# Optimization experiments

Measured on AMD Instinct MI355X. Metric: run time of the kernel, lower is better.

Reference implementation:

```python
import jax, jax.numpy as jnp
import numpy as np

B, S, H, L, NH, FF, V, NL = 16, 512, 768, 12, 12, 3072, 30522, 9
DH = H // NH


def setup_inputs() -> dict:
    key = jax.random.key(0)
    ks = iter(jax.random.split(key, 16))
    def w(shape, scale=0.02):
        return jax.random.normal(next(ks), shape, jnp.float32) * scale
    return {
        "input_word_ids": jax.random.randint(next(ks), (B, S), 0, V, jnp.int32),
        "input_mask": jnp.ones((B, S), jnp.int32),
        "input_type_ids": jnp.zeros((B, S), jnp.int32),
        "valid_mask": jax.random.randint(next(ks), (B, S), 0, 2, jnp.int32),
        "word_emb": w((V, H)),
        "pos_emb": w((S, H)),
        "type_emb": w((2, H)),
        "emb_ln_g": jnp.ones((H,), jnp.float32),
        "emb_ln_b": jnp.zeros((H,), jnp.float32),
        "Wq": w((L, H, H)), "bq": jnp.zeros((L, H), jnp.float32),
        "Wk": w((L, H, H)), "bk": jnp.zeros((L, H), jnp.float32),
        "Wv": w((L, H, H)), "bv": jnp.zeros((L, H), jnp.float32),
        "Wo": w((L, H, H)), "bo": jnp.zeros((L, H), jnp.float32),
        "ln1_g": jnp.ones((L, H), jnp.float32), "ln1_b": jnp.zeros((L, H), jnp.float32),
        "W1": w((L, H, FF)), "b1": jnp.zeros((L, FF), jnp.float32),
        "W2": w((L, FF, H)), "b2": jnp.zeros((L, H), jnp.float32),
        "ln2_g": jnp.ones((L, H), jnp.float32), "ln2_b": jnp.zeros((L, H), jnp.float32),
        "cls_W": w((H, NL)), "cls_b": jnp.zeros((NL,), jnp.float32),
    }


def _layer_norm(x, g, b):
    m = x.mean(-1, keepdims=True)
    v = ((x - m) ** 2).mean(-1, keepdims=True)
    return (x - m) * jax.lax.rsqrt(v + 1e-12) * g + b


def reference(input_word_ids, input_mask, input_type_ids, valid_mask,
              word_emb, pos_emb, type_emb, emb_ln_g, emb_ln_b,
              Wq, bq, Wk, bk, Wv, bv, Wo, bo, ln1_g, ln1_b,
              W1, b1, W2, b2, ln2_g, ln2_b, cls_W, cls_b):
    b, s = input_word_ids.shape
    # --- BERT embeddings ---
    x = word_emb[input_word_ids] + pos_emb[None, :s] + type_emb[input_type_ids]
    x = _layer_norm(x, emb_ln_g, emb_ln_b)  # [B,S,H]
    attn_bias = (1.0 - input_mask.astype(jnp.float32))[:, None, None, :] * -1e9
    scale = 1.0 / np.sqrt(DH).astype(np.float32)

    def step(h, p):
        wq, bq_, wk, bk_, wv, bv_, wo, bo_, g1, gb1, w1, wb1, w2, wb2, g2, gb2 = p
        q = (h @ wq + bq_).reshape(b, s, NH, DH)
        k = (h @ wk + bk_).reshape(b, s, NH, DH)
        v = (h @ wv + bv_).reshape(b, s, NH, DH)
        scores = jnp.einsum('bqhd,bkhd->bhqk', q, k) * scale + attn_bias
        probs = jax.nn.softmax(scores, axis=-1)
        ctx = jnp.einsum('bhqk,bkhd->bqhd', probs, v).reshape(b, s, H)
        h = _layer_norm(h + ctx @ wo + bo_, g1, gb1)
        ff = jax.nn.gelu(h @ w1 + wb1, approximate=False)
        h = _layer_norm(h + ff @ w2 + wb2, g2, gb2)
        return h, None

    params = (Wq, bq, Wk, bk, Wv, bv, Wo, bo, ln1_g, ln1_b, W1, b1, W2, b2, ln2_g, ln2_b)
    x, _ = jax.lax.scan(step, x, params)

    # --- valid-token compaction (vectorized form of the python double loop) ---
    # valid tokens packed to the front (stable order), remainder zero-padded
    invalid = (1 - valid_mask).astype(jnp.int32)
    perm = jnp.argsort(invalid, axis=1, stable=True)          # [B,S]
    compact = jnp.take_along_axis(x, perm[:, :, None], axis=1)
    counts = valid_mask.sum(axis=1)                           # [B]
    keep = (jnp.arange(s)[None, :] < counts[:, None])[:, :, None]
    compact = jnp.where(keep, compact, jnp.zeros((), x.dtype))
    # dropout is identity at inference (training=False)
    logits = jax.nn.softmax(compact @ cls_W + cls_b, axis=-1)  # [B,S,NL]
    return logits
```

## Files before the change

### kernel.cpp

```cpp
#include <hip/hip_runtime.h>
#include <cstdint>
#include <cstddef>

#define B_ 16
#define S_ 512
#define H_ 768
#define L_ 12
#define NH_ 12
#define DH_ 64
#define FF_ 3072
#define NL_ 9
#define QKV_ 2304

typedef _Float16 f16x8 __attribute__((ext_vector_type(8)));
typedef _Float16 f16x4 __attribute__((ext_vector_type(4)));
typedef float f32x4 __attribute__((ext_vector_type(4)));

__device__ __forceinline__ void load_lds16(const void* g, void* l) {
  __builtin_amdgcn_global_load_lds(
      (const __attribute__((address_space(1))) unsigned int*)g,
      (__attribute__((address_space(3))) unsigned int*)l, 16, 0, 0);
}

__device__ __forceinline__ float block_sum256(float v, float* red) {
#pragma unroll
  for (int off = 32; off; off >>= 1) v += __shfl_down(v, off);
  __syncthreads();
  if ((threadIdx.x & 63) == 0) red[threadIdx.x >> 6] = v;
  __syncthreads();
  return red[0] + red[1] + red[2] + red[3];
}

__device__ __forceinline__ float block_sum192(float v, float* red) {
#pragma unroll
  for (int off = 32; off; off >>= 1) v += __shfl_down(v, off);
  __syncthreads();
  if ((threadIdx.x & 63) == 0) red[threadIdx.x >> 6] = v;
  __syncthreads();
  return red[0] + red[1] + red[2];
}

__device__ __forceinline__ float gelu_f(float x) {
  float au = fabsf(x) * 0.70710678118654752f;
  float t = 1.0f / (1.0f + 0.3275911f * au);
  float p = ((((1.061405429f * t - 1.453152027f) * t + 1.421413741f) * t
              - 0.284496736f) * t + 0.254829592f) * t;
  float e = p * __expf(-au * au);
  float phi = (x >= 0.0f) ? (1.0f - 0.5f * e) : (0.5f * e);
  return x * phi;
}

__global__ __launch_bounds__(256) void embed_ln_kernel(
    const int* __restrict__ wid, const int* __restrict__ tpid,
    const float* __restrict__ we, const float* __restrict__ pe,
    const float* __restrict__ te, const float* __restrict__ g,
    const float* __restrict__ bb, _Float16* __restrict__ hb) {
  __shared__ float red[4];
  int tok = blockIdx.x;
  int s = tok & (S_ - 1);
  int w = wid[tok], tp = tpid[tok];
  int t = threadIdx.x;
  float x[3];
#pragma unroll
  for (int i = 0; i < 3; ++i) {
    int j = t + i * 256;
    x[i] = we[(size_t)w * H_ + j] + pe[(size_t)s * H_ + j] + te[(size_t)tp * H_ + j];
  }
  float m = block_sum256(x[0] + x[1] + x[2], red) * (1.0f / H_);
  float d0 = x[0] - m, d1 = x[1] - m, d2 = x[2] - m;
  float var = block_sum256(d0 * d0 + d1 * d1 + d2 * d2, red) * (1.0f / H_);
  float rs = rsqrtf(var + 1e-12f);
#pragma unroll
  for (int i = 0; i < 3; ++i) {
    int j = t + i * 256;
    float v = (x[i] - m) * rs * g[j] + bb[j];
    hb[(size_t)tok * H_ + j] = (_Float16)v;
  }
}

__global__ __launch_bounds__(192) void ln_f16_kernel(
    const _Float16* __restrict__ x, const float* __restrict__ g,
    const float* __restrict__ bb, _Float16* __restrict__ hb) {
  __shared__ float red[3];
  int tok = blockIdx.x;
  int t = threadIdx.x;
  int j = t * 4;
  f16x4 xv = *(const f16x4*)&x[(size_t)tok * H_ + j];
  float v0 = (float)xv[0], v1 = (float)xv[1], v2 = (float)xv[2], v3 = (float)xv[3];
  float m = block_sum192(v0 + v1 + v2 + v3, red) * (1.0f / H_);
  float d0 = v0 - m, d1 = v1 - m, d2 = v2 - m, d3 = v3 - m;
  __syncthreads();
  float var = block_sum192(d0 * d0 + d1 * d1 + d2 * d2 + d3 * d3, red) * (1.0f / H_);
  float rs = rsqrtf(var + 1e-12f);
  float4 gv = *(const float4*)&g[j];
  float4 bv = *(const float4*)&bb[j];
  f16x4 o;
  o[0] = (_Float16)(d0 * rs * gv.x + bv.x);
  o[1] = (_Float16)(d1 * rs * gv.y + bv.y);
  o[2] = (_Float16)(d2 * rs * gv.z + bv.z);
  o[3] = (_Float16)(d3 * rs * gv.w + bv.w);
  *(f16x4*)&hb[(size_t)tok * H_ + j] = o;
}

__global__ __launch_bounds__(256) void convert_weights_kernel(
    const float* __restrict__ Wq, const float* __restrict__ Wk,
    const float* __restrict__ Wv, const float* __restrict__ Wo,
    const float* __restrict__ W1, const float* __restrict__ W2,
    _Float16* __restrict__ qT, _Float16* __restrict__ kT,
    _Float16* __restrict__ vT, _Float16* __restrict__ oT,
    _Float16* __restrict__ w1T, _Float16* __restrict__ w2T,
    const float* __restrict__ bq, const float* __restrict__ bk,
    const float* __restrict__ bv, float* __restrict__ qkvb) {
  int id = blockIdx.x;
  int tid = threadIdx.x;
  if (id == 1728) {
    for (int j = tid; j < H_; j += 256) {
      qkvb[j] = bq[j];
      qkvb[H_ + j] = bk[j];
      qkvb[2 * H_ + j] = bv[j];
    }
    return;
  }
  __shared__ float T[64][65];
  const float* src;
  _Float16* dst;
  int K, N, tk, tn;
  if (id < 576) {
    int mat = id / 144, t = id % 144;
    K = 768; N = 768; tk = t / 12; tn = t % 12;
    src = (mat == 0) ? Wq : (mat == 1) ? Wk : (mat == 2) ? Wv : Wo;
    dst = (mat == 0) ? qT : (mat == 1) ? kT : (mat == 2) ? vT : oT;
  } else if (id < 1152) {
    int t = id - 576; K = 768; N = 3072; tk = t / 48; tn = t % 48;
    src = W1; dst = w1T;
  } else {
    int t = id - 1152; K = 3072; N = 768; tk = t / 12; tn = t % 12;
    src = W2; dst = w2T;
  }
  int k0 = tk * 64, n0 = tn * 64;
  {
    int r = tid >> 4, c4 = (tid & 15) * 4;
#pragma unroll
    for (int i = 0; i < 4; ++i) {
      float4 v = *(const float4*)&src[(size_t)(k0 + r + i * 16) * N + n0 + c4];
      T[r + i * 16][c4 + 0] = v.x;
      T[r + i * 16][c4 + 1] = v.y;
      T[r + i * 16][c4 + 2] = v.z;
      T[r + i * 16][c4 + 3] = v.w;
    }
  }
  __syncthreads();
#pragma unroll
  for (int i = 0; i < 2; ++i) {
    int chunk = tid + i * 256;
    int n = chunk >> 3, kc = (chunk & 7) * 8;
    f16x8 o;
#pragma unroll
    for (int j = 0; j < 8; ++j) o[j] = (_Float16)T[kc + j][n];
    *(f16x8*)&dst[(size_t)(n0 + n) * K + k0 + kc] = o;
  }
}

template <int OUT>
__global__ __launch_bounds__(256) void gemm_f16(
    const _Float16* __restrict__ A, const _Float16* __restrict__ Bt,
    const float* __restrict__ bias, void* __restrict__ Cv,
    int M, int N, int K, const _Float16* __restrict__ hres) {
  __shared__ _Float16 As[2][128 * 64];
  __shared__ _Float16 Bs[2][128 * 64];
  int tid = threadIdx.x;
  int lane = tid & 63, w = tid >> 6;
  int wr = w >> 1, wc = w & 1;
  int l15 = lane & 15, kb = lane >> 4;
  int swr = l15 & 7;

  int nwg = gridDim.x * gridDim.y;
  int bid = blockIdx.y * gridDim.x + blockIdx.x;
  int swz = bid;
  if ((nwg & 7) == 0) {
    int cpx = nwg >> 3;
    swz = (bid & 7) * cpx + (bid >> 3);
  }
  int bx = swz % gridDim.x, by = swz / gridDim.x;
  int row0 = by * 128, col0 = bx * 128;

  int drow = lane >> 3;
  int schunk = (lane & 7) ^ drow;
  const _Float16* gA = A + (size_t)(row0 + w * 32 + drow) * K + schunk * 8;
  const _Float16* gB = Bt + (size_t)(col0 + w * 32 + drow) * K + schunk * 8;

  auto STAGE = [&](int t, int buf) {
    int ko = t * 64;
#pragma unroll
    for (int j = 0; j < 4; ++j) {
      load_lds16(gA + (size_t)(j * 8) * K + ko,
                 (char*)&As[buf][0] + (w * 32 + j * 8) * 128);
      load_lds16(gB + (size_t)(j * 8) * K + ko,
                 (char*)&Bs[buf][0] + (w * 32 + j * 8) * 128);
    }
  };

  f32x4 acc[4][4] = {};
  int nk = K >> 6;

  STAGE(0, 0);
  __syncthreads();

  for (int kt = 0; kt < nk; ++kt) {
    int cur = kt & 1;
    if (kt + 1 < nk) STAGE(kt + 1, cur ^ 1);
#pragma unroll
    for (int ks = 0; ks < 2; ++ks) {
      f16x8 af[4], bf[4];
      int rpos = ((ks * 4 + kb) ^ swr) * 8;
#pragma unroll
      for (int m = 0; m < 4; ++m)
        af[m] = *(const f16x8*)&As[cur][(wr * 64 + m * 16 + l15) * 64 + rpos];
#pragma unroll
      for (int n = 0; n < 4; ++n)
        bf[n] = *(const f16x8*)&Bs[cur][(wc * 64 + n * 16 + l15) * 64 + rpos];
#pragma unroll
      for (int m = 0; m < 4; ++m)
#pragma unroll
        for (int n = 0; n < 4; ++n)
          acc[m][n] = __builtin_amdgcn_mfma_f32_16x16x32_f16(af[m], bf[n], acc[m][n], 0, 0, 0);
    }
    __syncthreads();
  }
#pragma unroll
  for (int n = 0; n < 4; ++n) {
    int col = col0 + wc * 64 + n * 16 + l15;
    float bv = bias[col];
#pragma unroll
    for (int m = 0; m < 4; ++m) {
      int rowb = row0 + wr * 64 + m * 16 + kb * 4;
#pragma unroll
      for (int r = 0; r < 4; ++r) {
        float v = acc[m][n][r] + bv;
        if (OUT == 2) v = gelu_f(v);
        if (OUT == 3) v += (float)hres[(size_t)(rowb + r) * N + col];
        ((_Float16*)Cv)[(size_t)(rowb + r) * N + col] = (_Float16)v;
      }
    }
  }
}

__global__ __launch_bounds__(256) void vtrans_kernel(
    const _Float16* __restrict__ v, int RS, _Float16* __restrict__ vt) {
  __shared__ _Float16 T[64][72];
  int s0 = blockIdx.x * 64;
  int bh = blockIdx.y;
  int b = bh / NH_, h = bh % NH_;
  int tid = threadIdx.x;
#pragma unroll
  for (int i = 0; i < 2; ++i) {
    int chunk = tid + i * 256;
    int s = chunk >> 3, dc = (chunk & 7) * 8;
    *(f16x8*)&T[s][dc] = *(const f16x8*)&v[(size_t)(b * S_ + s0 + s) * RS + h * DH_ + dc];
  }
  __syncthreads();
#pragma unroll
  for (int i = 0; i < 2; ++i) {
    int chunk = tid + i * 256;
    int d = chunk >> 3, sc = (chunk & 7) * 8;
    f16x8 o;
#pragma unroll
    for (int j = 0; j < 8; ++j) o[j] = T[sc + j][d];
    *(f16x8*)&vt[(size_t)(bh * DH_ + d) * S_ + s0 + sc] = o;
  }
}

__global__ __launch_bounds__(256) void flash_attn_kernel(
    const _Float16* __restrict__ q, const _Float16* __restrict__ k,
    const _Float16* __restrict__ vt, int RS, const int* __restrict__ mask,
    _Float16* __restrict__ ctx) {
  __shared__ _Float16 Ks[128 * 72];
  __shared__ _Float16 Vs[64 * 136];
  __shared__ _Float16 Ps[4][16 * 136];
  __shared__ float biasz[S_];
  int qt = blockIdx.x, h = blockIdx.y, b = blockIdx.z;
  int tid = threadIdx.x, lane = tid & 63, w = tid >> 6;
  int l15 = lane & 15, kb = lane >> 4;
  const float C = 0.125f * 1.44269504088896f;

  for (int i = tid; i < S_; i += 256)
    biasz[i] = (1.0f - (float)mask[b * S_ + i]) * (-1e9f * C);

  int qrow = b * S_ + qt * 64 + w * 16 + l15;
  f16x8 qf[2];
  qf[0] = *(const f16x8*)&q[(size_t)qrow * RS + h * DH_ + kb * 8];
  qf[1] = *(const f16x8*)&q[(size_t)qrow * RS + h * DH_ + 32 + kb * 8];

  auto loadKV = [&](int kt, f16x8* rk, f16x8* rv) {
#pragma unroll
    for (int i = 0; i < 4; ++i) {
      int idx = tid + i * 256;
      int r = idx >> 3, c = idx & 7;
      rk[i] = *(const f16x8*)&k[(size_t)(b * S_ + kt * 128 + r) * RS + h * DH_ + c * 8];
      int d = idx >> 4, c2 = idx & 15;
      rv[i] = *(const f16x8*)&vt[(size_t)((b * NH_ + h) * DH_ + d) * S_ + kt * 128 + c2 * 8];
    }
  };

  float m_run[4], l_run[4];
  f32x4 o[4] = {};
#pragma unroll
  for (int r = 0; r < 4; ++r) { m_run[r] = -1e30f; l_run[r] = 0.f; }

  f16x8 rk[4], rv[4];
  loadKV(0, rk, rv);
  for (int kt = 0; kt < 4; ++kt) {
    __syncthreads();
#pragma unroll
    for (int i = 0; i < 4; ++i) {
      int idx = tid + i * 256;
      int r = idx >> 3, c = idx & 7;
      *(f16x8*)&Ks[r * 72 + c * 8] = rk[i];
      int d = idx >> 4, c2 = idx & 15;
      *(f16x8*)&Vs[d * 136 + c2 * 8] = rv[i];
    }
    __syncthreads();
    if (kt < 3) loadKV(kt + 1, rk, rv);
    f32x4 s[8];
#pragma unroll
    for (int nf = 0; nf < 8; ++nf) {
      f16x8 b0 = *(const f16x8*)&Ks[(nf * 16 + l15) * 72 + kb * 8];
      f16x8 b1 = *(const f16x8*)&Ks[(nf * 16 + l15) * 72 + 32 + kb * 8];
      f32x4 z = {};
      z = __builtin_amdgcn_mfma_f32_16x16x32_f16(qf[0], b0, z, 0, 0, 0);
      z = __builtin_amdgcn_mfma_f32_16x16x32_f16(qf[1], b1, z, 0, 0, 0);
      s[nf] = z;
    }
    float zb[8];
#pragma unroll
    for (int nf = 0; nf < 8; ++nf) zb[nf] = biasz[kt * 128 + nf * 16 + l15];
    float pw[8][4];
    float corr[4];
#pragma unroll
    for (int r = 0; r < 4; ++r) {
      float mx = -1e30f;
#pragma unroll
      for (int nf = 0; nf < 8; ++nf) mx = fmaxf(mx, s[nf][r] * C + zb[nf]);
#pragma unroll
      for (int d = 1; d < 16; d <<= 1) mx = fmaxf(mx, __shfl_xor(mx, d));
      float mnew = fmaxf(m_run[r], mx);
      float cr = exp2f(m_run[r] - mnew);
      m_run[r] = mnew;
      corr[r] = cr;
      float sum = 0.f;
#pragma unroll
      for (int nf = 0; nf < 8; ++nf) {
        float pv = exp2f(s[nf][r] * C + zb[nf] - mnew);
        pw[nf][r] = pv;
        sum += pv;
      }
#pragma unroll
      for (int d = 1; d < 16; d <<= 1) sum += __shfl_xor(sum, d);
      l_run[r] = l_run[r] * cr + sum;
    }
#pragma unroll
    for (int nf2 = 0; nf2 < 4; ++nf2)
#pragma unroll
      for (int r = 0; r < 4; ++r) o[nf2][r] *= corr[r];
#pragma unroll
    for (int nf = 0; nf < 8; ++nf)
#pragma unroll
      for (int r = 0; r < 4; ++r)
        Ps[w][(kb * 4 + r) * 136 + nf * 16 + l15] = (_Float16)pw[nf][r];
#pragma unroll
    for (int ks = 0; ks < 4; ++ks) {
      f16x8 pa = *(const f16x8*)&Ps[w][l15 * 136 + ks * 32 + kb * 8];
#pragma unroll
      for (int nf2 = 0; nf2 < 4; ++nf2) {
        f16x8 vb2 = *(const f16x8*)&Vs[(nf2 * 16 + l15) * 136 + ks * 32 + kb * 8];
        o[nf2] = __builtin_amdgcn_mfma_f32_16x16x32_f16(pa, vb2, o[nf2], 0, 0, 0);
      }
    }
  }
  float inv[4];
#pragma unroll
  for (int r = 0; r < 4; ++r) inv[r] = 1.0f / fmaxf(l_run[r], 1e-37f);
#pragma unroll
  for (int nf2 = 0; nf2 < 4; ++nf2)
#pragma unroll
    for (int r = 0; r < 4; ++r) {
      int row = b * S_ + qt * 64 + w * 16 + kb * 4 + r;
      ctx[(size_t)row * H_ + h * DH_ + nf2 * 16 + l15] = (_Float16)(o[nf2][r] * inv[r]);
    }
}

__global__ void compact_idx_kernel(const int* __restrict__ valid, int* __restrict__ dest) {
  int b = threadIdx.x;
  if (b >= B_) return;
  int cnt = 0;
  for (int s = 0; s < S_; ++s) {
    int vv = valid[b * S_ + s];
    dest[b * S_ + s] = vv ? cnt : -1;
    cnt += vv;
  }
}

__global__ __launch_bounds__(192) void scatter_kernel(
    const _Float16* __restrict__ hb, const int* __restrict__ dest,
    float* __restrict__ compact) {
  int tok = blockIdx.x;
  int d = dest[tok];
  if (d < 0) return;
  int b = tok >> 9;
  int j = threadIdx.x * 4;
  f16x4 v = *(const f16x4*)&hb[(size_t)tok * H_ + j];
  float4 o = {(float)v[0], (float)v[1], (float)v[2], (float)v[3]};
  *(float4*)&compact[((size_t)(b * S_ + d)) * H_ + j] = o;
}

__global__ __launch_bounds__(256) void cls_kernel(
    const float* __restrict__ x, const float* __restrict__ W,
    const float* __restrict__ bias2, float* __restrict__ out) {
  int lane = threadIdx.x & 63, wv = threadIdx.x >> 6;
  int tok = blockIdx.x * 4 + wv;
  float acc[NL_] = {};
  for (int hh = lane; hh < H_; hh += 64) {
    float xv = x[(size_t)tok * H_ + hh];
#pragma unroll
    for (int n = 0; n < NL_; ++n) acc[n] = fmaf(xv, W[hh * NL_ + n], acc[n]);
  }
#pragma unroll
  for (int n = 0; n < NL_; ++n) {
#pragma unroll
    for (int off = 32; off; off >>= 1) acc[n] += __shfl_down(acc[n], off);
  }
  if (lane == 0) {
    float vls[NL_], mx = -1e30f;
#pragma unroll
    for (int n = 0; n < NL_; ++n) {
      vls[n] = acc[n] + bias2[n];
      mx = fmaxf(mx, vls[n]);
    }
    float s = 0.f;
#pragma unroll
    for (int n = 0; n < NL_; ++n) {
      vls[n] = expf(vls[n] - mx);
      s += vls[n];
    }
    float inv = 1.0f / s;
#pragma unroll
    for (int n = 0; n < NL_; ++n) out[(size_t)tok * NL_ + n] = vls[n] * inv;
  }
}

extern "C" void kernel_launch(void* const* d_in, const int* in_sizes, int n_in,
                              void* d_out, int out_size, void* d_ws, size_t ws_size,
                              hipStream_t stream) {
  const int* wid = (const int*)d_in[0];
  const int* mask = (const int*)d_in[1];
  const int* tpid = (const int*)d_in[2];
  const int* valid = (const int*)d_in[3];
  const float* we = (const float*)d_in[4];
  const float* pe = (const float*)d_in[5];
  const float* te = (const float*)d_in[6];
  const float* eg = (const float*)d_in[7];
  const float* eb = (const float*)d_in[8];
  const float* Wq = (const float*)d_in[9];
  const float* bq = (const float*)d_in[10];
  const float* Wk = (const float*)d_in[11];
  const float* bk = (const float*)d_in[12];
  const float* Wv = (const float*)d_in[13];
  const float* bv = (const float*)d_in[14];
  const float* Wo = (const float*)d_in[15];
  const float* bo = (const float*)d_in[16];
  const float* g1 = (const float*)d_in[17];
  const float* gb1 = (const float*)d_in[18];
  const float* W1 = (const float*)d_in[19];
  const float* bf1 = (const float*)d_in[20];
  const float* W2 = (const float*)d_in[21];
  const float* bf2 = (const float*)d_in[22];
  const float* g2 = (const float*)d_in[23];
  const float* gb2 = (const float*)d_in[24];
  const float* cW = (const float*)d_in[25];
  const float* cb = (const float*)d_in[26];
  float* out = (float*)d_out;

  const size_t TOK = (size_t)B_ * S_;
  char* ws = (char*)d_ws;
  _Float16* hb = (_Float16*)(ws + 25165824);
  _Float16* t1h = (_Float16*)(ws + 37748736);
  char* un1 = ws + 62914560;
  _Float16* qkv = (_Float16*)un1;
  _Float16* vt = (_Float16*)(un1 + 37748736);
  _Float16* ffh = (_Float16*)un1;
  float* compactf = (float*)un1;
  _Float16* ctx = (_Float16*)(ws + 113246208);
  char* wbuf = ws + 125829120;
  _Float16* wqT = (_Float16*)wbuf;
  _Float16* wkT = (_Float16*)(wbuf + 1179648);
  _Float16* wvT = (_Float16*)(wbuf + 2359296);
  _Float16* woT = (_Float16*)(wbuf + 3538944);
  _Float16* w1T = (_Float16*)(wbuf + 4718592);
  _Float16* w2T = (_Float16*)(wbuf + 9437184);
  int* dest = (int*)(ws + 139984896);
  float* qkvb = (float*)(ws + 140017664);

  dim3 blk(256);
  dim3 blk192(192);
  embed_ln_kernel<<<dim3((unsigned)TOK), blk, 0, stream>>>(wid, tpid, we, pe, te, eg, eb, hb);

  dim3 gQKV(QKV_ / 128, TOK / 128);
  dim3 gH(H_ / 128, TOK / 128);
  dim3 gF(FF_ / 128, TOK / 128);
  for (int l = 0; l < L_; ++l) {
    convert_weights_kernel<<<dim3(1729), blk, 0, stream>>>(
        Wq + (size_t)l * H_ * H_, Wk + (size_t)l * H_ * H_,
        Wv + (size_t)l * H_ * H_, Wo + (size_t)l * H_ * H_,
        W1 + (size_t)l * H_ * FF_, W2 + (size_t)l * FF_ * H_,
        wqT, wkT, wvT, woT, w1T, w2T,
        bq + l * H_, bk + l * H_, bv + l * H_, qkvb);
    gemm_f16<1><<<gQKV, blk, 0, stream>>>(hb, wqT, qkvb, qkv, (int)TOK, QKV_, H_, nullptr);
    vtrans_kernel<<<dim3(S_ / 64, B_ * NH_), blk, 0, stream>>>(qkv + 2 * H_, QKV_, vt);
    flash_attn_kernel<<<dim3(S_ / 64, NH_, B_), blk, 0, stream>>>(
        qkv, qkv + H_, vt, QKV_, mask, ctx);
    gemm_f16<3><<<gH, blk, 0, stream>>>(ctx, woT, bo + l * H_, t1h, (int)TOK, H_, H_, hb);
    ln_f16_kernel<<<dim3((unsigned)TOK), blk192, 0, stream>>>(t1h, g1 + l * H_, gb1 + l * H_, hb);
    gemm_f16<2><<<gF, blk, 0, stream>>>(hb, w1T, bf1 + l * FF_, ffh, (int)TOK, FF_, H_, nullptr);
    gemm_f16<3><<<gH, blk, 0, stream>>>(ffh, w2T, bf2 + l * H_, t1h, (int)TOK, H_, FF_, hb);
    ln_f16_kernel<<<dim3((unsigned)TOK), blk192, 0, stream>>>(t1h, g2 + l * H_, gb2 + l * H_, hb);
  }

  compact_idx_kernel<<<1, 64, 0, stream>>>(valid, dest);
  hipMemsetAsync(compactf, 0, TOK * H_ * sizeof(float), stream);
  scatter_kernel<<<dim3((unsigned)TOK), blk192, 0, stream>>>(hb, dest, compactf);
  cls_kernel<<<dim3((unsigned)(TOK / 4)), blk, 0, stream>>>(compactf, cW, cb, out);
}
```

Before: 3.431 ms.

## Use 64x128 GEMM tiles, precompute mask bias, fuse compaction into classifier gather

GEMM tiles shrink from 128x128 with 4 waves to 64x128 with 2 waves per block, each wave owning a 64-column slice. This doubles the grid size, which helps occupancy and tail behaviour, at the cost of less A/B reuse per block. The attention mask bias is now computed once by its own kernel instead of in every attention block. The final compaction drops the fp32 memset and scatter: the classifier reads each fp16 hidden row through a gather index and treats padded rows as zero.

```diff
diff --git a/kernel.cpp b/kernel.cpp
--- a/kernel.cpp
+++ b/kernel.cpp
@@ -14,6 +14,7 @@
 
 typedef _Float16 f16x8 __attribute__((ext_vector_type(8)));
 typedef _Float16 f16x4 __attribute__((ext_vector_type(4)));
+typedef _Float16 f16x2 __attribute__((ext_vector_type(2)));
 typedef float f32x4 __attribute__((ext_vector_type(4)));
 
 __device__ __forceinline__ void load_lds16(const void* g, void* l) {
@@ -161,16 +162,21 @@
   }
 }
 
+__global__ void maskbias_kernel(const int* __restrict__ mask, float* __restrict__ bz) {
+  int i = blockIdx.x * 256 + threadIdx.x;
+  const float C = 0.125f * 1.44269504088896f;
+  bz[i] = (1.0f - (float)mask[i]) * (-1e9f * C);
+}
+
 template <int OUT>
-__global__ __launch_bounds__(256) void gemm_f16(
+__global__ __launch_bounds__(128) void gemm64(
     const _Float16* __restrict__ A, const _Float16* __restrict__ Bt,
     const float* __restrict__ bias, void* __restrict__ Cv,
     int M, int N, int K, const _Float16* __restrict__ hres) {
-  __shared__ _Float16 As[2][128 * 64];
+  __shared__ _Float16 As[2][64 * 64];
   __shared__ _Float16 Bs[2][128 * 64];
   int tid = threadIdx.x;
   int lane = tid & 63, w = tid >> 6;
-  int wr = w >> 1, wc = w & 1;
   int l15 = lane & 15, kb = lane >> 4;
   int swr = l15 & 7;
 
@@ -182,22 +188,23 @@
     swz = (bid & 7) * cpx + (bid >> 3);
   }
   int bx = swz % gridDim.x, by = swz / gridDim.x;
-  int row0 = by * 128, col0 = bx * 128;
+  int row0 = by * 64, col0 = bx * 128;
 
   int drow = lane >> 3;
   int schunk = (lane & 7) ^ drow;
   const _Float16* gA = A + (size_t)(row0 + w * 32 + drow) * K + schunk * 8;
-  const _Float16* gB = Bt + (size_t)(col0 + w * 32 + drow) * K + schunk * 8;
+  const _Float16* gB = Bt + (size_t)(col0 + w * 64 + drow) * K + schunk * 8;
 
   auto STAGE = [&](int t, int buf) {
     int ko = t * 64;
 #pragma unroll
-    for (int j = 0; j < 4; ++j) {
+    for (int j = 0; j < 4; ++j)
       load_lds16(gA + (size_t)(j * 8) * K + ko,
                  (char*)&As[buf][0] + (w * 32 + j * 8) * 128);
+#pragma unroll
+    for (int j = 0; j < 8; ++j)
       load_lds16(gB + (size_t)(j * 8) * K + ko,
-                 (char*)&Bs[buf][0] + (w * 32 + j * 8) * 128);
-    }
+                 (char*)&Bs[buf][0] + (w * 64 + j * 8) * 128);
   };
 
   f32x4 acc[4][4] = {};
@@ -215,10 +222,10 @@
       int rpos = ((ks * 4 + kb) ^ swr) * 8;
 #pragma unroll
       for (int m = 0; m < 4; ++m)
-        af[m] = *(const f16x8*)&As[cur][(wr * 64 + m * 16 + l15) * 64 + rpos];
+        af[m] = *(const f16x8*)&As[cur][(m * 16 + l15) * 64 + rpos];
 #pragma unroll
       for (int n = 0; n < 4; ++n)
-        bf[n] = *(const f16x8*)&Bs[cur][(wc * 64 + n * 16 + l15) * 64 + rpos];
+        bf[n] = *(const f16x8*)&Bs[cur][(w * 64 + n * 16 + l15) * 64 + rpos];
 #pragma unroll
       for (int m = 0; m < 4; ++m)
 #pragma unroll
@@ -229,11 +236,11 @@
   }
 #pragma unroll
   for (int n = 0; n < 4; ++n) {
-    int col = col0 + wc * 64 + n * 16 + l15;
+    int col = col0 + w * 64 + n * 16 + l15;
     float bv = bias[col];
 #pragma unroll
     for (int m = 0; m < 4; ++m) {
-      int rowb = row0 + wr * 64 + m * 16 + kb * 4;
+      int rowb = row0 + m * 16 + kb * 4;
 #pragma unroll
       for (int r = 0; r < 4; ++r) {
         float v = acc[m][n][r] + bv;
@@ -272,7 +279,7 @@
 
 __global__ __launch_bounds__(256) void flash_attn_kernel(
     const _Float16* __restrict__ q, const _Float16* __restrict__ k,
-    const _Float16* __restrict__ vt, int RS, const int* __restrict__ mask,
+    const _Float16* __restrict__ vt, int RS, const float* __restrict__ biasz_g,
     _Float16* __restrict__ ctx) {
   __shared__ _Float16 Ks[128 * 72];
   __shared__ _Float16 Vs[64 * 136];
@@ -283,8 +290,7 @@
   int l15 = lane & 15, kb = lane >> 4;
   const float C = 0.125f * 1.44269504088896f;
 
-  for (int i = tid; i < S_; i += 256)
-    biasz[i] = (1.0f - (float)mask[b * S_ + i]) * (-1e9f * C);
+  for (int i = tid; i < S_; i += 256) biasz[i] = biasz_g[b * S_ + i];
 
   int qrow = b * S_ + qt * 64 + w * 16 + l15;
   f16x8 qf[2];
@@ -389,40 +395,31 @@
     }
 }
 
-__global__ void compact_idx_kernel(const int* __restrict__ valid, int* __restrict__ dest) {
+__global__ void compact_idx_kernel(const int* __restrict__ valid, int* __restrict__ src_of) {
   int b = threadIdx.x;
   if (b >= B_) return;
   int cnt = 0;
-  for (int s = 0; s < S_; ++s) {
-    int vv = valid[b * S_ + s];
-    dest[b * S_ + s] = vv ? cnt : -1;
-    cnt += vv;
-  }
-}
-
-__global__ __launch_bounds__(192) void scatter_kernel(
-    const _Float16* __restrict__ hb, const int* __restrict__ dest,
-    float* __restrict__ compact) {
-  int tok = blockIdx.x;
-  int d = dest[tok];
-  if (d < 0) return;
-  int b = tok >> 9;
-  int j = threadIdx.x * 4;
-  f16x4 v = *(const f16x4*)&hb[(size_t)tok * H_ + j];
-  float4 o = {(float)v[0], (float)v[1], (float)v[2], (float)v[3]};
-  *(float4*)&compact[((size_t)(b * S_ + d)) * H_ + j] = o;
+  for (int s = 0; s < S_; ++s)
+    if (valid[b * S_ + s]) src_of[b * S_ + cnt++] = b * S_ + s;
+  for (int d = cnt; d < S_; ++d) src_of[b * S_ + d] = -1;
 }
 
 __global__ __launch_bounds__(256) void cls_kernel(
-    const float* __restrict__ x, const float* __restrict__ W,
-    const float* __restrict__ bias2, float* __restrict__ out) {
+    const _Float16* __restrict__ hb, const int* __restrict__ src_of,
+    const float* __restrict__ W, const float* __restrict__ bias2,
+    float* __restrict__ out) {
   int lane = threadIdx.x & 63, wv = threadIdx.x >> 6;
   int tok = blockIdx.x * 4 + wv;
+  int src = src_of[tok];
   float acc[NL_] = {};
-  for (int hh = lane; hh < H_; hh += 64) {
-    float xv = x[(size_t)tok * H_ + hh];
-#pragma unroll
-    for (int n = 0; n < NL_; ++n) acc[n] = fmaf(xv, W[hh * NL_ + n], acc[n]);
+  if (src >= 0) {
+    for (int h0 = lane * 2; h0 < H_; h0 += 128) {
+      f16x2 xv = *(const f16x2*)&hb[(size_t)src * H_ + h0];
+      float x0 = (float)xv[0], x1 = (float)xv[1];
+#pragma unroll
+      for (int n = 0; n < NL_; ++n)
+        acc[n] = fmaf(x0, W[h0 * NL_ + n], fmaf(x1, W[(h0 + 1) * NL_ + n], acc[n]));
+    }
   }
 #pragma unroll
   for (int n = 0; n < NL_; ++n) {
@@ -488,7 +485,6 @@
   _Float16* qkv = (_Float16*)un1;
   _Float16* vt = (_Float16*)(un1 + 37748736);
   _Float16* ffh = (_Float16*)un1;
-  float* compactf = (float*)un1;
   _Float16* ctx = (_Float16*)(ws + 113246208);
   char* wbuf = ws + 125829120;
   _Float16* wqT = (_Float16*)wbuf;
@@ -497,16 +493,19 @@
   _Float16* woT = (_Float16*)(wbuf + 3538944);
   _Float16* w1T = (_Float16*)(wbuf + 4718592);
   _Float16* w2T = (_Float16*)(wbuf + 9437184);
-  int* dest = (int*)(ws + 139984896);
+  int* src_of = (int*)(ws + 139984896);
   float* qkvb = (float*)(ws + 140017664);
+  float* biasz_g = (float*)(ws + 140026880);
 
   dim3 blk(256);
   dim3 blk192(192);
+  dim3 blk128(128);
   embed_ln_kernel<<<dim3((unsigned)TOK), blk, 0, stream>>>(wid, tpid, we, pe, te, eg, eb, hb);
-
-  dim3 gQKV(QKV_ / 128, TOK / 128);
-  dim3 gH(H_ / 128, TOK / 128);
-  dim3 gF(FF_ / 128, TOK / 128);
+  maskbias_kernel<<<dim3((unsigned)(TOK / 256)), blk, 0, stream>>>(mask, biasz_g);
+
+  dim3 gQKV64(QKV_ / 128, TOK / 64);
+  dim3 gH64(H_ / 128, TOK / 64);
+  dim3 gF64(FF_ / 128, TOK / 64);
   for (int l = 0; l < L_; ++l) {
     convert_weights_kernel<<<dim3(1729), blk, 0, stream>>>(
         Wq + (size_t)l * H_ * H_, Wk + (size_t)l * H_ * H_,
@@ -514,19 +513,17 @@
         W1 + (size_t)l * H_ * FF_, W2 + (size_t)l * FF_ * H_,
         wqT, wkT, wvT, woT, w1T, w2T,
         bq + l * H_, bk + l * H_, bv + l * H_, qkvb);
-    gemm_f16<1><<<gQKV, blk, 0, stream>>>(hb, wqT, qkvb, qkv, (int)TOK, QKV_, H_, nullptr);
+    gemm64<1><<<gQKV64, blk128, 0, stream>>>(hb, wqT, qkvb, qkv, (int)TOK, QKV_, H_, nullptr);
     vtrans_kernel<<<dim3(S_ / 64, B_ * NH_), blk, 0, stream>>>(qkv + 2 * H_, QKV_, vt);
     flash_attn_kernel<<<dim3(S_ / 64, NH_, B_), blk, 0, stream>>>(
-        qkv, qkv + H_, vt, QKV_, mask, ctx);
-    gemm_f16<3><<<gH, blk, 0, stream>>>(ctx, woT, bo + l * H_, t1h, (int)TOK, H_, H_, hb);
+        qkv, qkv + H_, vt, QKV_, biasz_g, ctx);
+    gemm64<3><<<gH64, blk128, 0, stream>>>(ctx, woT, bo + l * H_, t1h, (int)TOK, H_, H_, hb);
     ln_f16_kernel<<<dim3((unsigned)TOK), blk192, 0, stream>>>(t1h, g1 + l * H_, gb1 + l * H_, hb);
-    gemm_f16<2><<<gF, blk, 0, stream>>>(hb, w1T, bf1 + l * FF_, ffh, (int)TOK, FF_, H_, nullptr);
-    gemm_f16<3><<<gH, blk, 0, stream>>>(ffh, w2T, bf2 + l * H_, t1h, (int)TOK, H_, FF_, hb);
+    gemm64<2><<<gF64, blk128, 0, stream>>>(hb, w1T, bf1 + l * FF_, ffh, (int)TOK, FF_, H_, nullptr);
+    gemm64<3><<<gH64, blk128, 0, stream>>>(ffh, w2T, bf2 + l * H_, t1h, (int)TOK, H_, FF_, hb);
     ln_f16_kernel<<<dim3((unsigned)TOK), blk192, 0, stream>>>(t1h, g2 + l * H_, gb2 + l * H_, hb);
   }
 
-  compact_idx_kernel<<<1, 64, 0, stream>>>(valid, dest);
-  hipMemsetAsync(compactf, 0, TOK * H_ * sizeof(float), stream);
-  scatter_kernel<<<dim3((unsigned)TOK), blk192, 0, stream>>>(hb, dest, compactf);
-  cls_kernel<<<dim3((unsigned)(TOK / 4)), blk, 0, stream>>>(compactf, cW, cb, out);
-}
+  compact_idx_kernel<<<1, 64, 0, stream>>>(valid, src_of);
+  cls_kernel<<<dim3((unsigned)(TOK / 4)), blk, 0, stream>>>(hb, src_of, cW, cb, out);
+}
```

Result: slower. 3.638 ms (+6.0%).
